# Optimization experiments

Hardware: AMD Instinct MI355X
Metric: run time of the kernel (lower is better)

Reference implementation:

```python
import math
import jax, jax.numpy as jnp
import numpy as np

N_HEADS = 16
N_KV_HEADS = 4
HEAD_DIM = 64
DIM = 1024
WINDOW = 16
EPS = 0.01


def _alibi_slopes(n_heads):
    closest = 2 ** math.floor(math.log2(n_heads))
    base = 2.0 ** (-2.0 ** (-(math.log2(closest) - 3)))
    slopes = base ** np.arange(1, closest + 1, dtype=np.float32)
    if closest < n_heads:
        eb = 2.0 ** (-2.0 ** (-(math.log2(2 * closest) - 3)))
        extra = eb ** np.arange(1, 2 * (n_heads - closest) + 1, 2, dtype=np.float32)
        slopes = np.concatenate([slopes, extra])
    return jnp.asarray(slopes[:n_heads])


def _rmsnorm(x, w):
    xf = x.astype(jnp.float32)
    norm = jax.lax.rsqrt(jnp.mean(xf * xf, axis=-1, keepdims=True) + EPS)
    return (xf * norm).astype(x.dtype) * w


def setup_inputs() -> dict:
    key = jax.random.key(0)
    ks = jax.random.split(key, 6)
    B, L = 2, 2048
    s = 1.0 / math.sqrt(DIM)
    return {
        "x": jax.random.normal(ks[0], (B, L, DIM), jnp.float32),
        "wq": jax.random.normal(ks[1], (N_HEADS * HEAD_DIM, DIM), jnp.float32) * s,
        "wk": jax.random.normal(ks[2], (N_KV_HEADS * HEAD_DIM, DIM), jnp.float32) * s,
        "wv": jax.random.normal(ks[3], (N_KV_HEADS * HEAD_DIM, DIM), jnp.float32) * s,
        "wo": jax.random.normal(ks[4], (DIM, N_HEADS * HEAD_DIM), jnp.float32) * s,
        "q_norm_w": jnp.ones((HEAD_DIM,), jnp.float32),
        "k_norm_w": jnp.ones((HEAD_DIM,), jnp.float32),
    }


def reference(x, wq, wk, wv, wo, q_norm_w, k_norm_w):
    B, L, _ = x.shape
    n_rep = N_HEADS // N_KV_HEADS
    q = (x @ wq.T).reshape(B, L, N_HEADS, HEAD_DIM)
    k = (x @ wk.T).reshape(B, L, N_KV_HEADS, HEAD_DIM)
    v = (x @ wv.T).reshape(B, L, N_KV_HEADS, HEAD_DIM)
    q = _rmsnorm(q, q_norm_w)
    k = _rmsnorm(k, k_norm_w)
    # GQA repeat: head h maps to kv head (h % n_kv_heads), matching torch expand order
    k = jnp.broadcast_to(k[:, :, None], (B, L, n_rep, N_KV_HEADS, HEAD_DIM)).reshape(B, L, N_HEADS, HEAD_DIM)
    v = jnp.broadcast_to(v[:, :, None], (B, L, n_rep, N_KV_HEADS, HEAD_DIM)).reshape(B, L, N_HEADS, HEAD_DIM)
    # ALiBi bias with causal + sliding-window mask
    pos = jnp.arange(L)
    rel = pos[None, :] - pos[:, None]  # [L, L], j - i
    slopes = _alibi_slopes(N_HEADS)  # [H]
    bias = slopes[:, None, None] * rel[None].astype(jnp.float32)  # [H, L, L]
    masked = (rel > 0) | (rel < -WINDOW)
    bias = jnp.where(masked[None], -jnp.inf, bias)
    scale = 1.0 / math.sqrt(HEAD_DIM)
    attn = jnp.einsum("bqhd,bkhd->bhqk", q, k) * scale + bias[None]
    attn = jax.nn.softmax(attn, axis=-1)
    out = jnp.einsum("bhqk,bkhd->bqhd", attn, v).reshape(B, L, N_HEADS * HEAD_DIM)
    return out @ wo.T
```

## Files before the change

kernel.cpp:

```cpp
#include <hip/hip_runtime.h>
#include <math.h>

#define DIM 1024
#define NH 16
#define NKV 4
#define HD 64
#define WINDOW 16
#define EPS 0.01f

typedef __bf16 bf16_t;
typedef bf16_t bf16x8 __attribute__((ext_vector_type(8)));
typedef bf16_t bf16x4 __attribute__((ext_vector_type(4)));
typedef float f32x4 __attribute__((ext_vector_type(4)));

__global__ __launch_bounds__(256) void f2bf_all(const float* __restrict__ x,
                                                const float* __restrict__ wq,
                                                const float* __restrict__ wk,
                                                const float* __restrict__ wv,
                                                const float* __restrict__ wo,
                                                bf16_t* __restrict__ xb,
                                                bf16_t* __restrict__ wqkvb,
                                                bf16_t* __restrict__ wob) {
  int i = blockIdx.x * blockDim.x + threadIdx.x;
  const float* src;
  bf16_t* dst;
  int off;
  if (i < 1048576) { src = x; dst = xb; off = i; }
  else if (i < 1310720) { src = wq; dst = wqkvb; off = i - 1048576; }
  else if (i < 1376256) { src = wk; dst = wqkvb + (size_t)1024 * DIM; off = i - 1310720; }
  else if (i < 1441792) { src = wv; dst = wqkvb + (size_t)1280 * DIM; off = i - 1376256; }
  else { src = wo; dst = wob; off = i - 1441792; }
  float4 f = ((const float4*)src)[off];
  bf16x4 o = {(bf16_t)f.x, (bf16_t)f.y, (bf16_t)f.z, (bf16_t)f.w};
  ((bf16x4*)dst)[off] = o;
}


#define GEMM_BK64_LOOP(Aptr, Bptr)                                              \
  for (int k0 = 0; k0 < K; k0 += 64) {                                          \
    const bf16_t* Ag = Aptr + (size_t)row0 * K + k0;                            \
    const bf16_t* Bg = Bptr + (size_t)col0 * K + k0;                            \
    _Pragma("unroll")                                                           \
    for (int it = 0; it < 4; it++) {                                            \
      int c = it * 256 + t;                                                     \
      int r = c >> 3;                                                           \
      int kc = ((c & 7) - r) & 7;                                               \
      __builtin_amdgcn_global_load_lds(                                         \
          (const __attribute__((address_space(1))) void*)(Ag + (size_t)r * K + kc * 8), \
          (__attribute__((address_space(3))) void*)(As + c * 8), 16, 0, 0);     \
      __builtin_amdgcn_global_load_lds(                                         \
          (const __attribute__((address_space(1))) void*)(Bg + (size_t)r * K + kc * 8), \
          (__attribute__((address_space(3))) void*)(Bs + c * 8), 16, 0, 0);     \
    }                                                                           \
    __syncthreads();                                                            \
    _Pragma("unroll")                                                           \
    for (int h = 0; h < 2; h++) {                                               \
      bf16x8 af[4], bfr[4];                                                     \
      _Pragma("unroll")                                                         \
      for (int mi = 0; mi < 4; mi++) af[mi] = *(const bf16x8*)(As + aoff[h][mi]); \
      _Pragma("unroll")                                                         \
      for (int ni = 0; ni < 4; ni++) bfr[ni] = *(const bf16x8*)(Bs + boff[h][ni]); \
      _Pragma("unroll")                                                         \
      for (int mi = 0; mi < 4; mi++)                                            \
        _Pragma("unroll")                                                       \
        for (int ni = 0; ni < 4; ni++)                                          \
          acc[mi][ni] = __builtin_amdgcn_mfma_f32_16x16x32_bf16(af[mi], bfr[ni], \
                                                                acc[mi][ni], 0, 0, 0); \
    }                                                                           \
    __syncthreads();                                                            \
  }

#define GEMM_PROLOGUE()                                                         \
  const int t = threadIdx.x;                                                    \
  const int lane = t & 63;                                                      \
  const int wid = t >> 6;                                                       \
  const int row0 = blockIdx.y * 128;                                            \
  const int col0 = blockIdx.x * 128;                                            \
  const int wm = (wid >> 1) * 64;                                               \
  const int wn = (wid & 1) * 64;                                                \
  const int lquad = lane >> 4;                                                  \
  const int lcol = lane & 15;                                                   \
  int aoff[2][4], boff[2][4];                                                   \
  _Pragma("unroll")                                                             \
  for (int h = 0; h < 2; h++) {                                                 \
    _Pragma("unroll")                                                           \
    for (int mi = 0; mi < 4; mi++) {                                            \
      int r = wm + mi * 16 + lcol;                                              \
      aoff[h][mi] = r * 64 + (((h * 4 + lquad) + r) & 7) * 8;                   \
    }                                                                           \
    _Pragma("unroll")                                                           \
    for (int ni = 0; ni < 4; ni++) {                                            \
      int r = wn + ni * 16 + lcol;                                              \
      boff[h][ni] = r * 64 + (((h * 4 + lquad) + r) & 7) * 8;                   \
    }                                                                           \
  }                                                                             \
  f32x4 acc[4][4] = {};

__global__ __launch_bounds__(256) void gemm_qkv_rms(const bf16_t* __restrict__ A,
                                                    const bf16_t* __restrict__ B,
                                                    bf16_t* __restrict__ C,
                                                    const float* __restrict__ qw,
                                                    const float* __restrict__ kw,
                                                    int M, int N, int K) {
  __shared__ bf16_t As[128 * 64];
  __shared__ bf16_t Bs[128 * 64];
  GEMM_PROLOGUE()
  GEMM_BK64_LOOP(A, B)

  const int hcol = (col0 + wn) >> 6;
  const bool isv = (hcol >= 20);
  float wreg[4];
  if (!isv) {
    const float* wp = (hcol < 16) ? qw : kw;
#pragma unroll
    for (int ni = 0; ni < 4; ni++) wreg[ni] = wp[ni * 16 + lcol];
  }

#pragma unroll
  for (int mi = 0; mi < 4; mi++) {
#pragma unroll
    for (int r = 0; r < 4; r++) {
      float norm = 1.0f;
      if (!isv) {
        float ss = 0.0f;
#pragma unroll
        for (int ni = 0; ni < 4; ni++) ss += acc[mi][ni][r] * acc[mi][ni][r];
#pragma unroll
        for (int off = 8; off >= 1; off >>= 1) ss += __shfl_xor(ss, off);
        norm = rsqrtf(ss * (1.0f / 64.0f) + EPS);
      }
      size_t base = (size_t)(row0 + wm + mi * 16 + lquad * 4 + r) * N + col0 + wn + lcol;
#pragma unroll
      for (int ni = 0; ni < 4; ni++) {
        float v = acc[mi][ni][r] * norm;
        if (!isv) v *= wreg[ni];
        C[base + ni * 16] = (bf16_t)v;
      }
    }
  }
}

template <typename CT>
__global__ __launch_bounds__(256) void gemm_bf16(const bf16_t* __restrict__ A,
                                                 const bf16_t* __restrict__ B,
                                                 CT* __restrict__ C,
                                                 int M, int N, int K) {
  __shared__ bf16_t As[128 * 64];
  __shared__ bf16_t Bs[128 * 64];
  GEMM_PROLOGUE()
  GEMM_BK64_LOOP(A, B)

#pragma unroll
  for (int mi = 0; mi < 4; mi++)
#pragma unroll
    for (int ni = 0; ni < 4; ni++) {
      size_t base = (size_t)(row0 + wm + mi * 16 + lquad * 4) * N + col0 + wn + ni * 16 + lcol;
#pragma unroll
      for (int r = 0; r < 4; r++)
        C[base + (size_t)r * N] = (CT)acc[mi][ni][r];
    }
}

#define LKP 72
#define LVP 40

__global__ __launch_bounds__(256) void attn_mfma(const bf16_t* __restrict__ qkv,
                                                 bf16_t* __restrict__ y) {
  __shared__ bf16_t Ks[4][32][LKP];
  __shared__ bf16_t VTs[4][64][LVP];
  __shared__ bf16_t Ps[4][16][LVP];

  const int t = threadIdx.x;
  const int lane = t & 63;
  const int w = t >> 6;
  const int tile = blockIdx.x >> 2;
  const int hgroup = blockIdx.x & 3;
  const int b = tile >> 7;
  const int i0loc = (tile & 127) << 4;
  const int rowbase = b << 11;
  const int rowg0 = rowbase + i0loc;

#pragma unroll
  for (int it = 0; it < 4; it++) {
    int chunk = t + it * 256;
    int kvh = chunk >> 8;
    int key = (chunk >> 3) & 31;
    int dc = chunk & 7;
    int jloc = i0loc - 16 + key;
    int rg = rowbase + (jloc < 0 ? 0 : jloc);
    bf16x8 val = *(const bf16x8*)(qkv + (size_t)rg * 1536 + 1024 + kvh * 64 + dc * 8);
    *(bf16x8*)(&Ks[kvh][key][dc * 8]) = val;
  }
#pragma unroll
  for (int it = 0; it < 4; it++) {
    int idx = t + it * 256;
    int kvh = idx >> 8;
    int key = (idx >> 3) & 31;
    int dc = idx & 7;
    int jloc = i0loc - 16 + key;
    int rg = rowbase + (jloc < 0 ? 0 : jloc);
    bf16x8 val = *(const bf16x8*)(qkv + (size_t)rg * 1536 + 1280 + kvh * 64 + dc * 8);
    int kslot = ((key >> 3) ^ (dc & 3)) * 8 + (key & 7);
#pragma unroll
    for (int e = 0; e < 8; e++) VTs[kvh][dc * 8 + e][kslot] = val[e];
  }
  __syncthreads();

  const int col = lane & 15;
  const int quad = lane >> 4;
  const int h = hgroup * 4 + w;
  const int kvh = w;
  const float slope = exp2f(-0.5f * (float)(h + 1));

  bf16x8 kf[2][2];
#pragma unroll
  for (int kt = 0; kt < 2; kt++)
#pragma unroll
    for (int kc = 0; kc < 2; kc++)
      kf[kt][kc] = *(const bf16x8*)(&Ks[kvh][kt * 16 + col][kc * 32 + quad * 8]);
  bf16x8 vf[4];
#pragma unroll
  for (int nt = 0; nt < 4; nt++) {
    int dim = nt * 16 + col;
    int kchunk = quad ^ ((dim >> 3) & 3);
    vf[nt] = *(const bf16x8*)(&VTs[kvh][dim][kchunk * 8]);
  }

  const bf16_t* qrow = qkv + (size_t)(rowg0 + col) * 1536 + h * 64;
  bf16x8 qf0 = *(const bf16x8*)(qrow + quad * 8);
  bf16x8 qf1 = *(const bf16x8*)(qrow + 32 + quad * 8);

  f32x4 s0 = {}, s1 = {};
  s0 = __builtin_amdgcn_mfma_f32_16x16x32_bf16(qf0, kf[0][0], s0, 0, 0, 0);
  s0 = __builtin_amdgcn_mfma_f32_16x16x32_bf16(qf1, kf[0][1], s0, 0, 0, 0);
  s1 = __builtin_amdgcn_mfma_f32_16x16x32_bf16(qf0, kf[1][0], s1, 0, 0, 0);
  s1 = __builtin_amdgcn_mfma_f32_16x16x32_bf16(qf1, kf[1][1], s1, 0, 0, 0);

  const bool t0dead = (i0loc == 0);
  float sc0[4], sc1[4];
#pragma unroll
  for (int r = 0; r < 4; r++) {
    int rel0 = col - 16 - (quad * 4 + r);
    int rel1 = rel0 + 16;
    bool m0 = t0dead || (rel0 < -WINDOW);
    bool m1 = (rel1 > 0);
    sc0[r] = m0 ? -INFINITY : s0[r] * 0.125f + slope * (float)rel0;
    sc1[r] = m1 ? -INFINITY : s1[r] * 0.125f + slope * (float)rel1;
  }
  float mx[4], sum[4], p0[4], p1[4];
#pragma unroll
  for (int r = 0; r < 4; r++) mx[r] = fmaxf(sc0[r], sc1[r]);
#pragma unroll
  for (int off = 8; off >= 1; off >>= 1)
#pragma unroll
    for (int r = 0; r < 4; r++) mx[r] = fmaxf(mx[r], __shfl_xor(mx[r], off));
#pragma unroll
  for (int r = 0; r < 4; r++) {
    p0[r] = __expf(sc0[r] - mx[r]);
    p1[r] = __expf(sc1[r] - mx[r]);
    sum[r] = p0[r] + p1[r];
  }
#pragma unroll
  for (int off = 8; off >= 1; off >>= 1)
#pragma unroll
    for (int r = 0; r < 4; r++) sum[r] += __shfl_xor(sum[r], off);

#pragma unroll
  for (int r = 0; r < 4; r++) {
    Ps[w][quad * 4 + r][col] = (bf16_t)p0[r];
    Ps[w][quad * 4 + r][16 + col] = (bf16_t)p1[r];
  }
  __syncthreads();
  bf16x8 pf = *(const bf16x8*)(&Ps[w][col][quad * 8]);

  f32x4 o[4] = {};
#pragma unroll
  for (int nt = 0; nt < 4; nt++)
    o[nt] = __builtin_amdgcn_mfma_f32_16x16x32_bf16(pf, vf[nt], o[nt], 0, 0, 0);

#pragma unroll
  for (int nt = 0; nt < 4; nt++)
#pragma unroll
    for (int r = 0; r < 4; r++)
      y[(size_t)(rowg0 + quad * 4 + r) * 1024 + h * 64 + nt * 16 + col] =
          (bf16_t)(o[nt][r] / sum[r]);
}

extern "C" void kernel_launch(void* const* d_in, const int* in_sizes, int n_in,
                              void* d_out, int out_size, void* d_ws, size_t ws_size,
                              hipStream_t stream) {
  const float* x  = (const float*)d_in[0];
  const float* wq = (const float*)d_in[1];
  const float* wk = (const float*)d_in[2];
  const float* wv = (const float*)d_in[3];
  const float* wo = (const float*)d_in[4];
  const float* qw = (const float*)d_in[5];
  const float* kw = (const float*)d_in[6];
  float* out = (float*)d_out;

  const int M = 4096;

  bf16_t* xb    = (bf16_t*)d_ws;
  bf16_t* wqkvb = xb + (size_t)M * DIM;
  bf16_t* wob   = wqkvb + (size_t)1536 * DIM;
  bf16_t* qkv   = wob + (size_t)DIM * DIM;
  bf16_t* yb    = qkv + (size_t)M * 1536;

  dim3 blk(256);
  f2bf_all<<<1703936 / 256, blk, 0, stream>>>(x, wq, wk, wv, wo, xb, wqkvb, wob);

  gemm_qkv_rms<<<dim3(1536 / 128, M / 128), blk, 0, stream>>>(xb, wqkvb, qkv, qw, kw, M, 1536, DIM);

  attn_mfma<<<1024, blk, 0, stream>>>(qkv, yb);

  gemm_bf16<float><<<dim3(DIM / 128, M / 128), blk, 0, stream>>>(yb, wob, out, M, DIM, DIM);
}
```

Baseline: 145.6 us.

## Double-buffer GEMM LDS tiles to overlap global loads with MFMA compute

The GEMM main loop now holds two LDS buffers for the A and B tiles. While the MFMAs work on the current K-slice, the global_load_lds for the next slice is issued into the other buffer, and only one barrier is needed per iteration instead of two. The aim is to hide global-memory latency behind matrix math in both the QKV+RMSNorm GEMM and the output projection GEMM. The cost is double the shared memory per block (64KB), which may cut the number of resident blocks per CU.

```diff
diff --git a/kernel.cpp b/kernel.cpp
--- a/kernel.cpp
+++ b/kernel.cpp
@@ -36,38 +36,49 @@
 }
 
 
-#define GEMM_BK64_LOOP(Aptr, Bptr)                                              \
-  for (int k0 = 0; k0 < K; k0 += 64) {                                          \
-    const bf16_t* Ag = Aptr + (size_t)row0 * K + k0;                            \
-    const bf16_t* Bg = Bptr + (size_t)col0 * K + k0;                            \
+#define GEMM_STAGE(buf, Ag, Bg)                                                 \
+  {                                                                             \
     _Pragma("unroll")                                                           \
     for (int it = 0; it < 4; it++) {                                            \
       int c = it * 256 + t;                                                     \
       int r = c >> 3;                                                           \
       int kc = ((c & 7) - r) & 7;                                               \
       __builtin_amdgcn_global_load_lds(                                         \
-          (const __attribute__((address_space(1))) void*)(Ag + (size_t)r * K + kc * 8), \
-          (__attribute__((address_space(3))) void*)(As + c * 8), 16, 0, 0);     \
+          (const __attribute__((address_space(1))) void*)((Ag) + (size_t)r * K + kc * 8), \
+          (__attribute__((address_space(3))) void*)(As[buf] + c * 8), 16, 0, 0); \
       __builtin_amdgcn_global_load_lds(                                         \
-          (const __attribute__((address_space(1))) void*)(Bg + (size_t)r * K + kc * 8), \
-          (__attribute__((address_space(3))) void*)(Bs + c * 8), 16, 0, 0);     \
+          (const __attribute__((address_space(1))) void*)((Bg) + (size_t)r * K + kc * 8), \
+          (__attribute__((address_space(3))) void*)(Bs[buf] + c * 8), 16, 0, 0); \
     }                                                                           \
-    __syncthreads();                                                            \
-    _Pragma("unroll")                                                           \
-    for (int h = 0; h < 2; h++) {                                               \
-      bf16x8 af[4], bfr[4];                                                     \
+  }
+
+#define GEMM_DBUF_LOOP(Aptr, Bptr)                                              \
+  {                                                                             \
+    const bf16_t* Abase = Aptr + (size_t)row0 * K;                              \
+    const bf16_t* Bbase = Bptr + (size_t)col0 * K;                              \
+    GEMM_STAGE(0, Abase, Bbase)                                                 \
+    const int nIter = K >> 6;                                                   \
+    for (int ki = 0; ki < nIter; ki++) {                                        \
+      __syncthreads();                                                          \
+      if (ki + 1 < nIter)                                                       \
+        GEMM_STAGE((ki + 1) & 1, Abase + (ki + 1) * 64, Bbase + (ki + 1) * 64)  \
+      const bf16_t* Ab = As[ki & 1];                                            \
+      const bf16_t* Bb = Bs[ki & 1];                                            \
       _Pragma("unroll")                                                         \
-      for (int mi = 0; mi < 4; mi++) af[mi] = *(const bf16x8*)(As + aoff[h][mi]); \
-      _Pragma("unroll")                                                         \
-      for (int ni = 0; ni < 4; ni++) bfr[ni] = *(const bf16x8*)(Bs + boff[h][ni]); \
-      _Pragma("unroll")                                                         \
-      for (int mi = 0; mi < 4; mi++)                                            \
+      for (int h = 0; h < 2; h++) {                                             \
+        bf16x8 af[4], bfr[4];                                                   \
         _Pragma("unroll")                                                       \
-        for (int ni = 0; ni < 4; ni++)                                          \
-          acc[mi][ni] = __builtin_amdgcn_mfma_f32_16x16x32_bf16(af[mi], bfr[ni], \
-                                                                acc[mi][ni], 0, 0, 0); \
+        for (int mi = 0; mi < 4; mi++) af[mi] = *(const bf16x8*)(Ab + aoff[h][mi]); \
+        _Pragma("unroll")                                                       \
+        for (int ni = 0; ni < 4; ni++) bfr[ni] = *(const bf16x8*)(Bb + boff[h][ni]); \
+        _Pragma("unroll")                                                       \
+        for (int mi = 0; mi < 4; mi++)                                          \
+          _Pragma("unroll")                                                     \
+          for (int ni = 0; ni < 4; ni++)                                        \
+            acc[mi][ni] = __builtin_amdgcn_mfma_f32_16x16x32_bf16(af[mi], bfr[ni], \
+                                                                  acc[mi][ni], 0, 0, 0); \
+      }                                                                         \
     }                                                                           \
-    __syncthreads();                                                            \
   }
 
 #define GEMM_PROLOGUE()                                                         \
@@ -102,10 +113,10 @@
                                                     const float* __restrict__ qw,
                                                     const float* __restrict__ kw,
                                                     int M, int N, int K) {
-  __shared__ bf16_t As[128 * 64];
-  __shared__ bf16_t Bs[128 * 64];
+  __shared__ bf16_t As[2][128 * 64];
+  __shared__ bf16_t Bs[2][128 * 64];
   GEMM_PROLOGUE()
-  GEMM_BK64_LOOP(A, B)
+  GEMM_DBUF_LOOP(A, B)
 
   const int hcol = (col0 + wn) >> 6;
   const bool isv = (hcol >= 20);
@@ -145,10 +156,10 @@
                                                  const bf16_t* __restrict__ B,
                                                  CT* __restrict__ C,
                                                  int M, int N, int K) {
-  __shared__ bf16_t As[128 * 64];
-  __shared__ bf16_t Bs[128 * 64];
+  __shared__ bf16_t As[2][128 * 64];
+  __shared__ bf16_t Bs[2][128 * 64];
   GEMM_PROLOGUE()
-  GEMM_BK64_LOOP(A, B)
+  GEMM_DBUF_LOOP(A, B)
 
 #pragma unroll
   for (int mi = 0; mi < 4; mi++)
```

After: 139.9 us. -3.9%, faster.
